# Optimization experiments

Measured on AMD Instinct MI355X. Metric: run time of the kernel, lower is better.

The kernel has to match this reference:

```python
import jax, jax.numpy as jnp
import numpy as np

N = 1048576
FEAT = 32
XRES = 512
TRES = 64
HID = 256
OUT = 2


def _bilinear_sample(plane, gx, gy):
    """plane: [C,H,W]; gx,gy: [N] in [-1,1] (x indexes W, y indexes H).
    Matches torch grid_sample(mode='bilinear', align_corners=True, padding_mode='zeros')
    for in-range coords. Returns [N,C]."""
    C, H, W = plane.shape
    ix = (gx + 1.0) * 0.5 * (W - 1)
    iy = (gy + 1.0) * 0.5 * (H - 1)
    x0f = jnp.floor(ix)
    y0f = jnp.floor(iy)
    wx = ix - x0f  # frac weights (grad flows to coords through ix)
    wy = iy - y0f
    x0 = jnp.clip(x0f.astype(jnp.int32), 0, W - 1)
    x1 = jnp.clip(x0 + 1, 0, W - 1)
    y0 = jnp.clip(y0f.astype(jnp.int32), 0, H - 1)
    y1 = jnp.clip(y0 + 1, 0, H - 1)
    v00 = plane[:, y0, x0]  # [C,N]
    v01 = plane[:, y0, x1]
    v10 = plane[:, y1, x0]
    v11 = plane[:, y1, x1]
    out = (v00 * ((1 - wx) * (1 - wy)) + v01 * (wx * (1 - wy))
           + v10 * ((1 - wx) * wy) + v11 * (wx * wy))
    return out.T  # [N,C]


def setup_inputs() -> dict:
    key = jax.random.key(0)
    ks = jax.random.split(key, 12)
    coords = jax.random.uniform(ks[0], (N, 3), jnp.float32, minval=-1.0, maxval=1.0)
    xy_plane = jax.random.normal(ks[1], (FEAT, XRES, XRES), jnp.float32) * 0.001
    yt_plane = jax.random.normal(ks[2], (FEAT, TRES, XRES), jnp.float32) * 0.001
    xt_plane = jax.random.normal(ks[3], (FEAT, TRES, XRES), jnp.float32) * 0.001
    def lin(kw, kb, fan_in, fan_out):
        bound = 1.0 / np.sqrt(fan_in)
        w = jax.random.uniform(kw, (fan_in, fan_out), jnp.float32, -bound, bound)
        b = jax.random.uniform(kb, (fan_out,), jnp.float32, -bound, bound)
        return w, b
    w1, b1 = lin(ks[4], ks[5], FEAT, HID)
    w2, b2 = lin(ks[6], ks[7], HID, HID)
    w3, b3 = lin(ks[8], ks[9], HID, HID)
    w4, b4 = lin(ks[10], ks[11], HID, OUT)
    return {"coordinates": coords, "xy_plane": xy_plane, "yt_plane": yt_plane,
            "xt_plane": xt_plane, "w1": w1, "b1": b1, "w2": w2, "b2": b2,
            "w3": w3, "b3": b3, "w4": w4, "b4": b4}


def reference(coordinates, xy_plane, yt_plane, xt_plane,
              w1, b1, w2, b2, w3, b3, w4, b4):
    x, y, t = coordinates[:, 0], coordinates[:, 1], coordinates[:, 2]
    # coords[...,0:2] -> xy plane; coords[...,1:3] -> yt plane; coords[...,::2] -> xt plane
    feats = (_bilinear_sample(xy_plane, x, y)
             + _bilinear_sample(yt_plane, y, t)
             + _bilinear_sample(xt_plane, x, t))  # [N, FEAT]
    h = jax.nn.leaky_relu(feats @ w1 + b1, 0.01)
    h = jax.nn.leaky_relu(h @ w2 + b2, 0.01)
    h = jax.nn.leaky_relu(h @ w3 + b3, 0.01)
    out = jax.nn.sigmoid(h @ w4 + b4)  # [N, OUT]
    return out
```

## Files before the change

### kernel.cpp

```cpp
#include <hip/hip_runtime.h>

typedef unsigned short u16;
typedef float f32x4 __attribute__((ext_vector_type(4)));
typedef short short8 __attribute__((ext_vector_type(8)));
typedef short short4v __attribute__((ext_vector_type(4)));

#define XRES 512
#define TRES 64

#define WS_XY 0
#define WS_YT 8388608
#define WS_XT 9437184
#define WS_WF 10485760
#define WF1 0
#define WF2 8192
#define WF3 73728
#define WS_NEEDED_BYTES 21250048ull

__device__ __forceinline__ u16 f2bf(float f) {
  union { float f; unsigned u; } v; v.f = f;
  unsigned r = v.u + 0x7FFFu + ((v.u >> 16) & 1u);
  return (u16)(r >> 16);
}
__device__ __forceinline__ float bf2f(u16 u) {
  union { unsigned u; float f; } v; v.u = ((unsigned)u) << 16;
  return v.f;
}

__device__ __forceinline__ f32x4 mfma16x16x32_bf16(short8 a, short8 b, f32x4 c) {
  f32x4 d;
  asm("v_mfma_f32_16x16x32_bf16 %0, %1, %2, %3" : "=v"(d) : "v"(a), "v"(b), "v"(c));
  return d;
}

__device__ __forceinline__ void sample_direct(const float* __restrict__ pl, int H, int W,
                                              float gx, float gy, float* acc) {
  float ix = (gx + 1.0f) * 0.5f * (float)(W - 1);
  float iy = (gy + 1.0f) * 0.5f * (float)(H - 1);
  float x0f = floorf(ix), y0f = floorf(iy);
  float wx = ix - x0f, wy = iy - y0f;
  int x0 = (int)x0f, y0 = (int)y0f;
  x0 = max(0, min(x0, W - 1)); y0 = max(0, min(y0, H - 1));
  int x1 = min(x0 + 1, W - 1), y1 = min(y0 + 1, H - 1);
  float w00 = (1.0f - wx) * (1.0f - wy), w01 = wx * (1.0f - wy);
  float w10 = (1.0f - wx) * wy,          w11 = wx * wy;
  const int HW = H * W;
  const int i00 = y0 * W + x0, i01 = y0 * W + x1, i10 = y1 * W + x0, i11 = y1 * W + x1;
#pragma unroll
  for (int c = 0; c < 32; ++c) {
    const float* pc = pl + c * HW;
    acc[c] += w00 * pc[i00] + w01 * pc[i01] + w10 * pc[i10] + w11 * pc[i11];
  }
}

__device__ void layer_valu(const float* hin, float* hout, const float* __restrict__ w,
                           const float* __restrict__ b) {
  for (int pass = 0; pass < 8; ++pass) {
    float acc[32];
#pragma unroll
    for (int jx = 0; jx < 32; ++jx) acc[jx] = b[pass * 32 + jx];
    for (int k = 0; k < 256; ++k) {
      const float hk = hin[k];
      const float* wr = w + k * 256 + pass * 32;
#pragma unroll
      for (int jx = 0; jx < 32; ++jx) acc[jx] = fmaf(hk, wr[jx], acc[jx]);
    }
#pragma unroll
    for (int jx = 0; jx < 32; ++jx) {
      float v = acc[jx];
      hout[pass * 32 + jx] = v > 0.f ? v : 0.01f * v;
    }
  }
}

__global__ void triplane_safe(const float* __restrict__ coords,
                              const float* __restrict__ xy, const float* __restrict__ yt,
                              const float* __restrict__ xt,
                              const float* __restrict__ w1, const float* __restrict__ b1,
                              const float* __restrict__ w2, const float* __restrict__ b2,
                              const float* __restrict__ w3, const float* __restrict__ b3,
                              const float* __restrict__ w4, const float* __restrict__ b4,
                              float* __restrict__ out) {
  const int pg = blockIdx.x * 256 + threadIdx.x;
  const float x  = coords[pg * 3 + 0];
  const float y  = coords[pg * 3 + 1];
  const float tt = coords[pg * 3 + 2];
  float feats[32];
#pragma unroll
  for (int c = 0; c < 32; ++c) feats[c] = 0.f;
  sample_direct(xy, XRES, XRES, x, y,  feats);
  sample_direct(yt, TRES, XRES, y, tt, feats);
  sample_direct(xt, TRES, XRES, x, tt, feats);

  float hA[256], hB[256];
  for (int pass = 0; pass < 8; ++pass) {
    float acc[32];
#pragma unroll
    for (int jx = 0; jx < 32; ++jx) acc[jx] = b1[pass * 32 + jx];
#pragma unroll
    for (int k = 0; k < 32; ++k) {
      const float fk = feats[k];
      const float* wr = w1 + k * 256 + pass * 32;
#pragma unroll
      for (int jx = 0; jx < 32; ++jx) acc[jx] = fmaf(fk, wr[jx], acc[jx]);
    }
#pragma unroll
    for (int jx = 0; jx < 32; ++jx) {
      float v = acc[jx];
      hA[pass * 32 + jx] = v > 0.f ? v : 0.01f * v;
    }
  }
  layer_valu(hA, hB, w2, b2);
  layer_valu(hB, hA, w3, b3);
  float a0 = b4[0], a1 = b4[1];
  for (int k = 0; k < 256; ++k) {
    a0 = fmaf(hA[k], w4[k * 2 + 0], a0);
    a1 = fmaf(hA[k], w4[k * 2 + 1], a1);
  }
  out[pg * 2 + 0] = 1.f / (1.f + __expf(-a0));
  out[pg * 2 + 1] = 1.f / (1.f + __expf(-a1));
}

__global__ void prep_planes(const float* __restrict__ xy, const float* __restrict__ yt,
                            const float* __restrict__ xt, u16* __restrict__ ws) {
  int i = blockIdx.x * 256 + threadIdx.x;
  const float* src; u16* dst; int HW; int idx;
  if (i < 262144)      { src = xy; dst = ws + WS_XY; HW = 262144; idx = i; }
  else if (i < 294912) { src = yt; dst = ws + WS_YT; HW = 32768;  idx = i - 262144; }
  else                 { src = xt; dst = ws + WS_XT; HW = 32768;  idx = i - 294912; }
  u16 tmp[32];
#pragma unroll
  for (int c = 0; c < 32; ++c) tmp[c] = f2bf(src[c * HW + idx]);
  short8* o = (short8*)(dst + (long)idx * 32);
#pragma unroll
  for (int s = 0; s < 4; ++s) o[s] = *(short8*)(tmp + s * 8);
}

__global__ void prep_weights(const float* __restrict__ w1, const float* __restrict__ w2,
                             const float* __restrict__ w3, u16* __restrict__ wf) {
  int tid = blockIdx.x * 256 + threadIdx.x;
  const float* src; int KS; int local; int dstbase;
  if (tid < 1024)      { src = w1; KS = 1; local = tid;        dstbase = WF1; }
  else if (tid < 9216) { src = w2; KS = 8; local = tid - 1024; dstbase = WF2; }
  else                 { src = w3; KS = 8; local = tid - 9216; dstbase = WF3; }
  int lane = local & 63, blk = local >> 6;
  int ks = blk % KS, CT = blk / KS;
  int col = CT * 16 + (lane & 15);
  int kb = ks * 32 + (lane >> 4) * 8;
  u16 tmp[8];
#pragma unroll
  for (int j = 0; j < 8; ++j) tmp[j] = f2bf(src[(kb + j) * 256 + col]);
  *(short8*)(wf + dstbase + local * 8) = *(short8*)tmp;
}

__device__ __forceinline__ void sample_plane4(const u16* __restrict__ pl, int H, int W,
                                              float gx, float gy, int c0, float* acc) {
  float ix = (gx + 1.0f) * 0.5f * (float)(W - 1);
  float iy = (gy + 1.0f) * 0.5f * (float)(H - 1);
  float x0f = floorf(ix), y0f = floorf(iy);
  float wx = ix - x0f, wy = iy - y0f;
  int x0 = (int)x0f, y0 = (int)y0f;
  x0 = max(0, min(x0, W - 1)); y0 = max(0, min(y0, H - 1));
  int x1 = min(x0 + 1, W - 1);
  int y1 = min(y0 + 1, H - 1);
  short4v v00 = *(const short4v*)(pl + (y0 * W + x0) * 32 + c0);
  short4v v01 = *(const short4v*)(pl + (y0 * W + x1) * 32 + c0);
  short4v v10 = *(const short4v*)(pl + (y1 * W + x0) * 32 + c0);
  short4v v11 = *(const short4v*)(pl + (y1 * W + x1) * 32 + c0);
  float w00 = (1.0f - wx) * (1.0f - wy), w01 = wx * (1.0f - wy);
  float w10 = (1.0f - wx) * wy,          w11 = wx * wy;
#pragma unroll
  for (int j = 0; j < 4; ++j)
    acc[j] += w00 * bf2f((u16)v00[j]) + w01 * bf2f((u16)v01[j])
            + w10 * bf2f((u16)v10[j]) + w11 * bf2f((u16)v11[j]);
}

template <int KSTEPS>
__device__ __forceinline__ void layer_gemm(const u16* src, u16* dst,
                                           const u16* __restrict__ wf,
                                           const float* __restrict__ bias,
                                           int wave, int lane) {
  const int r16 = lane & 15, kq = lane >> 4;
  f32x4 acc[2][4];
#pragma unroll
  for (int rt = 0; rt < 2; ++rt)
#pragma unroll
    for (int ct = 0; ct < 4; ++ct) acc[rt][ct] = (f32x4){0.f, 0.f, 0.f, 0.f};

  short8 aA[2], aB[2], bA[4], bB[4];

#define LDA(ks, dst_)                                                                   \
  {                                                                                     \
    const int kbyte_ = (ks) * 64 + kq * 16;                                             \
    _Pragma("unroll") for (int rt = 0; rt < 2; ++rt) {                                  \
      const int row_ = rt * 16 + r16;                                                   \
      dst_[rt] = *(const short8*)((const char*)src + row_ * 512 +                       \
                                  (kbyte_ ^ ((row_ & 7) << 4)));                        \
    }                                                                                   \
  }
#define LDB(ks, dst_)                                                                   \
  {                                                                                     \
    _Pragma("unroll") for (int ct = 0; ct < 4; ++ct)                                    \
        dst_[ct] = *(const short8*)(wf + (((wave * 4 + ct) * KSTEPS + (ks)) * 64 +      \
                                          lane) * 8);                                   \
  }

  LDA(0, aA); LDB(0, bA);
#pragma unroll
  for (int ks = 0; ks < KSTEPS; ++ks) {
    const bool even = (ks & 1) == 0;
    short8* ac = even ? aA : aB;
    short8* bc = even ? bA : bB;
    short8* an = even ? aB : aA;
    short8* bn = even ? bB : bA;
    if (ks + 1 < KSTEPS) { LDA(ks + 1, an); LDB(ks + 1, bn); }
#pragma unroll
    for (int rt = 0; rt < 2; ++rt)
#pragma unroll
      for (int ct = 0; ct < 4; ++ct)
        acc[rt][ct] = mfma16x16x32_bf16(ac[rt], bc[ct], acc[rt][ct]);
  }
#undef LDA
#undef LDB

#pragma unroll
  for (int ct = 0; ct < 4; ++ct) {
    const int col = wave * 64 + ct * 16 + r16;
    const float bv = bias[col];
#pragma unroll
    for (int rt = 0; rt < 2; ++rt)
#pragma unroll
      for (int q = 0; q < 4; ++q) {
        const int row = rt * 16 + kq * 4 + q;
        float v = acc[rt][ct][q] + bv;
        v = v > 0.f ? v : 0.01f * v;
        *(u16*)((char*)dst + row * 512 + ((col * 2) ^ ((row & 7) << 4))) = f2bf(v);
      }
  }
}

__global__ __launch_bounds__(256, 4) void triplane_fused(
    const float* __restrict__ coords, const u16* __restrict__ ws,
    const float* __restrict__ b1, const float* __restrict__ b2,
    const float* __restrict__ b3, const float* __restrict__ w4,
    const float* __restrict__ b4, float* __restrict__ out) {
  __shared__ u16 sA[32 * 256];
  __shared__ u16 sB[32 * 256];
  const int t = threadIdx.x;
  const int lane = t & 63, wave = t >> 6;
  const int pg0 = blockIdx.x * 32;

  {
    const int p = t >> 3, cg = t & 7, c0 = cg * 4;
    const int pg = pg0 + p;
    const float x  = coords[pg * 3 + 0];
    const float y  = coords[pg * 3 + 1];
    const float tt = coords[pg * 3 + 2];
    float acc4[4] = {0.f, 0.f, 0.f, 0.f};
    sample_plane4(ws + WS_XY, XRES, XRES, x, y,  c0, acc4);
    sample_plane4(ws + WS_YT, TRES, XRES, y, tt, c0, acc4);
    sample_plane4(ws + WS_XT, TRES, XRES, x, tt, c0, acc4);
    u16 packed[4];
#pragma unroll
    for (int j = 0; j < 4; ++j) packed[j] = f2bf(acc4[j]);
    *(short4v*)((char*)sA + p * 512 + ((c0 * 2) ^ ((p & 7) << 4))) = *(short4v*)packed;
  }
  __syncthreads();

  const u16* wfb = ws + WS_WF;
  layer_gemm<1>(sA, sB, wfb + WF1, b1, wave, lane);
  __syncthreads();
  layer_gemm<8>(sB, sA, wfb + WF2, b2, wave, lane);
  __syncthreads();
  layer_gemm<8>(sA, sB, wfb + WF3, b3, wave, lane);
  __syncthreads();

  {
    const int p = t >> 3, cg = t & 7;
    const int pg = pg0 + p;
    float a0 = 0.f, a1 = 0.f;
#pragma unroll
    for (int kk = 0; kk < 4; ++kk) {
      const int k0 = cg * 32 + kk * 8;
      short8 h = *(const short8*)((const char*)sB + p * 512 + ((k0 * 2) ^ ((p & 7) << 4)));
#pragma unroll
      for (int j = 0; j < 8; ++j) {
        const float hv = bf2f((u16)h[j]);
        a0 = fmaf(hv, w4[(k0 + j) * 2 + 0], a0);
        a1 = fmaf(hv, w4[(k0 + j) * 2 + 1], a1);
      }
    }
    a0 += __shfl_xor(a0, 1, 8); a0 += __shfl_xor(a0, 2, 8); a0 += __shfl_xor(a0, 4, 8);
    a1 += __shfl_xor(a1, 1, 8); a1 += __shfl_xor(a1, 2, 8); a1 += __shfl_xor(a1, 4, 8);
    if (cg == 0) {
      const float o0 = 1.f / (1.f + __expf(-(a0 + b4[0])));
      const float o1 = 1.f / (1.f + __expf(-(a1 + b4[1])));
      *(float2*)(out + pg * 2) = make_float2(o0, o1);
    }
  }
}

extern "C" void kernel_launch(void* const* d_in, const int* in_sizes, int n_in,
                              void* d_out, int out_size, void* d_ws, size_t ws_size,
                              hipStream_t stream) {
  (void)in_sizes; (void)n_in; (void)out_size;
  const float* coords = (const float*)d_in[0];
  const float* xy = (const float*)d_in[1];
  const float* yt = (const float*)d_in[2];
  const float* xt = (const float*)d_in[3];
  const float* w1 = (const float*)d_in[4];
  const float* b1 = (const float*)d_in[5];
  const float* w2 = (const float*)d_in[6];
  const float* b2 = (const float*)d_in[7];
  const float* w3 = (const float*)d_in[8];
  const float* b3 = (const float*)d_in[9];
  const float* w4 = (const float*)d_in[10];
  const float* b4 = (const float*)d_in[11];

  if (ws_size >= WS_NEEDED_BYTES && d_ws != nullptr) {
    u16* ws = (u16*)d_ws;
    prep_planes<<<1280, 256, 0, stream>>>(xy, yt, xt, ws);
    prep_weights<<<68, 256, 0, stream>>>(w1, w2, w3, ws + WS_WF);
    triplane_fused<<<32768, 256, 0, stream>>>(coords, ws, b1, b2, b3, w4, b4, (float*)d_out);
  } else {
    triplane_safe<<<4096, 256, 0, stream>>>(coords, xy, yt, xt, w1, b1, w2, b2, w3, b3, w4, b4,
                                            (float*)d_out);
  }
}
```

Before: 679.0 us.

## Double block to 64 points with 8 waves and retile layer GEMMs

Each block now handles 64 points with 512 threads instead of 32 points with 256 threads. The hidden-layer GEMM tile per wave changes from 32 rows × 64 columns to 64 rows × 32 columns, so each weight fragment is reused across more rows. The bias is folded into the accumulator initialisation, leaky ReLU becomes fmaxf, bf16 conversion uses the packed v_cvt_pk_bf16 instruction, and the MFMA uses the compiler builtin instead of inline asm. The price is double the LDS per block, which may limit occupancy, and the unseen parts of the kernel (later layers and output) must be consistent with 8 waves and 64 rows.

```diff
diff --git a/kernel.cpp b/kernel.cpp
--- a/kernel.cpp
+++ b/kernel.cpp
@@ -1,6 +1,7 @@
 #include <hip/hip_runtime.h>
 
 typedef unsigned short u16;
+typedef unsigned int u32;
 typedef float f32x4 __attribute__((ext_vector_type(4)));
 typedef short short8 __attribute__((ext_vector_type(8)));
 typedef short short4v __attribute__((ext_vector_type(4)));
@@ -26,11 +27,14 @@
   union { unsigned u; float f; } v; v.u = ((unsigned)u) << 16;
   return v.f;
 }
+__device__ __forceinline__ u32 cvtpk_bf16(float lo, float hi) {
+  u32 d;
+  asm("v_cvt_pk_bf16_f32 %0, %1, %2" : "=v"(d) : "v"(lo), "v"(hi));
+  return d;
+}
 
 __device__ __forceinline__ f32x4 mfma16x16x32_bf16(short8 a, short8 b, f32x4 c) {
-  f32x4 d;
-  asm("v_mfma_f32_16x16x32_bf16 %0, %1, %2, %3" : "=v"(d) : "v"(a), "v"(b), "v"(c));
-  return d;
+  return __builtin_amdgcn_mfma_f32_16x16x32_bf16(a, b, c, 0, 0, 0);
 }
 
 __device__ __forceinline__ void sample_direct(const float* __restrict__ pl, int H, int W,
@@ -181,18 +185,20 @@
                                            const float* __restrict__ bias,
                                            int wave, int lane) {
   const int r16 = lane & 15, kq = lane >> 4;
-  f32x4 acc[2][4];
-#pragma unroll
-  for (int rt = 0; rt < 2; ++rt)
-#pragma unroll
-    for (int ct = 0; ct < 4; ++ct) acc[rt][ct] = (f32x4){0.f, 0.f, 0.f, 0.f};
-
-  short8 aA[2], aB[2], bA[4], bB[4];
+  f32x4 acc[4][2];
+#pragma unroll
+  for (int ct = 0; ct < 2; ++ct) {
+    const float bv = bias[wave * 32 + ct * 16 + r16];
+#pragma unroll
+    for (int rt = 0; rt < 4; ++rt) acc[rt][ct] = (f32x4){bv, bv, bv, bv};
+  }
+
+  short8 aA[4], aB[4], bA[2], bB[2];
 
 #define LDA(ks, dst_)                                                                   \
   {                                                                                     \
     const int kbyte_ = (ks) * 64 + kq * 16;                                             \
-    _Pragma("unroll") for (int rt = 0; rt < 2; ++rt) {                                  \
+    _Pragma("unroll") for (int rt = 0; rt < 4; ++rt) {                                  \
       const int row_ = rt * 16 + r16;                                                   \
       dst_[rt] = *(const short8*)((const char*)src + row_ * 512 +                       \
                                   (kbyte_ ^ ((row_ & 7) << 4)));                        \
@@ -200,8 +206,8 @@
   }
 #define LDB(ks, dst_)                                                                   \
   {                                                                                     \
-    _Pragma("unroll") for (int ct = 0; ct < 4; ++ct)                                    \
-        dst_[ct] = *(const short8*)(wf + (((wave * 4 + ct) * KSTEPS + (ks)) * 64 +      \
+    _Pragma("unroll") for (int ct = 0; ct < 2; ++ct)                                    \
+        dst_[ct] = *(const short8*)(wf + (((wave * 2 + ct) * KSTEPS + (ks)) * 64 +      \
                                           lane) * 8);                                   \
   }
 
@@ -215,40 +221,45 @@
     short8* bn = even ? bB : bA;
     if (ks + 1 < KSTEPS) { LDA(ks + 1, an); LDB(ks + 1, bn); }
 #pragma unroll
-    for (int rt = 0; rt < 2; ++rt)
-#pragma unroll
-      for (int ct = 0; ct < 4; ++ct)
+    for (int rt = 0; rt < 4; ++rt)
+#pragma unroll
+      for (int ct = 0; ct < 2; ++ct)
         acc[rt][ct] = mfma16x16x32_bf16(ac[rt], bc[ct], acc[rt][ct]);
   }
 #undef LDA
 #undef LDB
 
 #pragma unroll
-  for (int ct = 0; ct < 4; ++ct) {
-    const int col = wave * 64 + ct * 16 + r16;
-    const float bv = bias[col];
-#pragma unroll
-    for (int rt = 0; rt < 2; ++rt)
-#pragma unroll
-      for (int q = 0; q < 4; ++q) {
-        const int row = rt * 16 + kq * 4 + q;
-        float v = acc[rt][ct][q] + bv;
-        v = v > 0.f ? v : 0.01f * v;
-        *(u16*)((char*)dst + row * 512 + ((col * 2) ^ ((row & 7) << 4))) = f2bf(v);
+  for (int ct = 0; ct < 2; ++ct) {
+    const int col = wave * 32 + ct * 16 + r16;
+#pragma unroll
+    for (int rt = 0; rt < 4; ++rt) {
+#pragma unroll
+      for (int qp = 0; qp < 2; ++qp) {
+        float v0 = acc[rt][ct][qp * 2 + 0];
+        float v1 = acc[rt][ct][qp * 2 + 1];
+        v0 = fmaxf(v0, 0.01f * v0);
+        v1 = fmaxf(v1, 0.01f * v1);
+        const u32 pk = cvtpk_bf16(v0, v1);
+        const int row0 = rt * 16 + kq * 4 + qp * 2;
+        const int row1 = row0 + 1;
+        *(u16*)((char*)dst + row0 * 512 + ((col * 2) ^ ((row0 & 7) << 4))) = (u16)pk;
+        *(u16*)((char*)dst + row1 * 512 + ((col * 2) ^ ((row1 & 7) << 4))) = (u16)(pk >> 16);
       }
-  }
-}
-
-__global__ __launch_bounds__(256, 4) void triplane_fused(
+    }
+  }
+}
+
+__global__ __launch_bounds__(512, 4) void triplane_fused(
     const float* __restrict__ coords, const u16* __restrict__ ws,
     const float* __restrict__ b1, const float* __restrict__ b2,
     const float* __restrict__ b3, const float* __restrict__ w4,
     const float* __restrict__ b4, float* __restrict__ out) {
-  __shared__ u16 sA[32 * 256];
-  __shared__ u16 sB[32 * 256];
+  __shared__ u16 sA[64 * 256];
+  __shared__ u16 sB[64 * 256];
   const int t = threadIdx.x;
   const int lane = t & 63, wave = t >> 6;
-  const int pg0 = blockIdx.x * 32;
+  const int pg0 = blockIdx.x * 64;
 
   {
     const int p = t >> 3, cg = t & 7, c0 = cg * 4;
@@ -321,7 +332,7 @@
     u16* ws = (u16*)d_ws;
     prep_planes<<<1280, 256, 0, stream>>>(xy, yt, xt, ws);
     prep_weights<<<68, 256, 0, stream>>>(w1, w2, w3, ws + WS_WF);
-    triplane_fused<<<32768, 256, 0, stream>>>(coords, ws, b1, b2, b3, w4, b4, (float*)d_out);
+    triplane_fused<<<16384, 512, 0, stream>>>(coords, ws, b1, b2, b3, w4, b4, (float*)d_out);
   } else {
     triplane_safe<<<4096, 256, 0, stream>>>(coords, xy, yt, xt, w1, b1, w2, b2, w3, b3, w4, b4,
                                             (float*)d_out);
```

After: 573.4 us. -15.6%, faster.

## Move final layer to MFMA, fold bias into accumulators, packed bf16 stores

Applied to the files above, without the earlier changes.

The 256-to-2 output layer now runs as a padded MFMA on two waves, using pre-converted bf16 w4 stored in the workspace, instead of scalar FMAs with shuffle reductions. Biases now initialise the accumulators instead of being added in the epilogue. Leaky-relu uses fmax and the bf16 conversion uses packed v_cvt_pk_bf16_f32. Layer-1 weights are prefetched before sampling to hide their load latency. The aim is to cut ALU and global-load work in the epilogues, at the cost of bf16 rounding in the last layer and idle waves there.

```diff
diff --git a/kernel.cpp b/kernel.cpp
--- a/kernel.cpp
+++ b/kernel.cpp
@@ -1,6 +1,7 @@
 #include <hip/hip_runtime.h>
 
 typedef unsigned short u16;
+typedef unsigned int u32;
 typedef float f32x4 __attribute__((ext_vector_type(4)));
 typedef short short8 __attribute__((ext_vector_type(8)));
 typedef short short4v __attribute__((ext_vector_type(4)));
@@ -15,7 +16,8 @@
 #define WF1 0
 #define WF2 8192
 #define WF3 73728
-#define WS_NEEDED_BYTES 21250048ull
+#define WF4 139264
+#define WS_NEEDED_BYTES 21258240ull
 
 __device__ __forceinline__ u16 f2bf(float f) {
   union { float f; unsigned u; } v; v.f = f;
@@ -26,11 +28,13 @@
   union { unsigned u; float f; } v; v.u = ((unsigned)u) << 16;
   return v.f;
 }
-
+__device__ __forceinline__ u32 cvtpk_bf16(float lo, float hi) {
+  u32 d;
+  asm("v_cvt_pk_bf16_f32 %0, %1, %2" : "=v"(d) : "v"(lo), "v"(hi));
+  return d;
+}
 __device__ __forceinline__ f32x4 mfma16x16x32_bf16(short8 a, short8 b, f32x4 c) {
-  f32x4 d;
-  asm("v_mfma_f32_16x16x32_bf16 %0, %1, %2, %3" : "=v"(d) : "v"(a), "v"(b), "v"(c));
-  return d;
+  return __builtin_amdgcn_mfma_f32_16x16x32_bf16(a, b, c, 0, 0, 0);
 }
 
 __device__ __forceinline__ void sample_direct(const float* __restrict__ pl, int H, int W,
@@ -137,20 +141,32 @@
 }
 
 __global__ void prep_weights(const float* __restrict__ w1, const float* __restrict__ w2,
-                             const float* __restrict__ w3, u16* __restrict__ wf) {
+                             const float* __restrict__ w3, const float* __restrict__ w4,
+                             u16* __restrict__ wf) {
   int tid = blockIdx.x * 256 + threadIdx.x;
-  const float* src; int KS; int local; int dstbase;
-  if (tid < 1024)      { src = w1; KS = 1; local = tid;        dstbase = WF1; }
-  else if (tid < 9216) { src = w2; KS = 8; local = tid - 1024; dstbase = WF2; }
-  else                 { src = w3; KS = 8; local = tid - 9216; dstbase = WF3; }
-  int lane = local & 63, blk = local >> 6;
-  int ks = blk % KS, CT = blk / KS;
-  int col = CT * 16 + (lane & 15);
-  int kb = ks * 32 + (lane >> 4) * 8;
-  u16 tmp[8];
-#pragma unroll
-  for (int j = 0; j < 8; ++j) tmp[j] = f2bf(src[(kb + j) * 256 + col]);
-  *(short8*)(wf + dstbase + local * 8) = *(short8*)tmp;
+  if (tid < 17408) {
+    const float* src; int KS; int local; int dstbase;
+    if (tid < 1024)      { src = w1; KS = 1; local = tid;        dstbase = WF1; }
+    else if (tid < 9216) { src = w2; KS = 8; local = tid - 1024; dstbase = WF2; }
+    else                 { src = w3; KS = 8; local = tid - 9216; dstbase = WF3; }
+    int lane = local & 63, blk = local >> 6;
+    int ks = blk % KS, CT = blk / KS;
+    int col = CT * 16 + (lane & 15);
+    int kb = ks * 32 + (lane >> 4) * 8;
+    u16 tmp[8];
+#pragma unroll
+    for (int j = 0; j < 8; ++j) tmp[j] = f2bf(src[(kb + j) * 256 + col]);
+    *(short8*)(wf + dstbase + local * 8) = *(short8*)tmp;
+  } else {
+    int local = tid - 17408;
+    int lane = local & 63, ks = local >> 6;
+    int col = lane & 15;
+    int kb = ks * 32 + (lane >> 4) * 8;
+    u16 tmp[8];
+#pragma unroll
+    for (int j = 0; j < 8; ++j) tmp[j] = (col < 2) ? f2bf(w4[(kb + j) * 2 + col]) : (u16)0;
+    *(short8*)(wf + WF4 + local * 8) = *(short8*)tmp;
+  }
 }
 
 __device__ __forceinline__ void sample_plane4(const u16* __restrict__ pl, int H, int W,
@@ -175,6 +191,29 @@
             + w10 * bf2f((u16)v10[j]) + w11 * bf2f((u16)v11[j]);
 }
 
+__device__ __forceinline__ void store_acts(f32x4 (&acc)[2][4], u16* dst, int wave,
+                                           int r16, int kq) {
+#pragma unroll
+  for (int ct = 0; ct < 4; ++ct) {
+    const int col = wave * 64 + ct * 16 + r16;
+#pragma unroll
+    for (int rt = 0; rt < 2; ++rt) {
+#pragma unroll
+      for (int qp = 0; qp < 2; ++qp) {
+        float v0 = acc[rt][ct][qp * 2 + 0];
+        float v1 = acc[rt][ct][qp * 2 + 1];
+        v0 = fmaxf(v0, 0.01f * v0);
+        v1 = fmaxf(v1, 0.01f * v1);
+        const u32 pk = cvtpk_bf16(v0, v1);
+        const int row0 = rt * 16 + kq * 4 + qp * 2;
+        const int row1 = row0 + 1;
+        *(u16*)((char*)dst + row0 * 512 + ((col * 2) ^ ((row0 & 7) << 4))) = (u16)pk;
+        *(u16*)((char*)dst + row1 * 512 + ((col * 2) ^ ((row1 & 7) << 4))) = (u16)(pk >> 16);
+      }
+    }
+  }
+}
+
 template <int KSTEPS>
 __device__ __forceinline__ void layer_gemm(const u16* src, u16* dst,
                                            const u16* __restrict__ wf,
@@ -183,9 +222,11 @@
   const int r16 = lane & 15, kq = lane >> 4;
   f32x4 acc[2][4];
 #pragma unroll
-  for (int rt = 0; rt < 2; ++rt)
-#pragma unroll
-    for (int ct = 0; ct < 4; ++ct) acc[rt][ct] = (f32x4){0.f, 0.f, 0.f, 0.f};
+  for (int ct = 0; ct < 4; ++ct) {
+    const float bv = bias[wave * 64 + ct * 16 + r16];
+#pragma unroll
+    for (int rt = 0; rt < 2; ++rt) acc[rt][ct] = (f32x4){bv, bv, bv, bv};
+  }
 
   short8 aA[2], aB[2], bA[4], bB[4];
 
@@ -223,32 +264,26 @@
 #undef LDA
 #undef LDB
 
-#pragma unroll
-  for (int ct = 0; ct < 4; ++ct) {
-    const int col = wave * 64 + ct * 16 + r16;
-    const float bv = bias[col];
-#pragma unroll
-    for (int rt = 0; rt < 2; ++rt)
-#pragma unroll
-      for (int q = 0; q < 4; ++q) {
-        const int row = rt * 16 + kq * 4 + q;
-        float v = acc[rt][ct][q] + bv;
-        v = v > 0.f ? v : 0.01f * v;
-        *(u16*)((char*)dst + row * 512 + ((col * 2) ^ ((row & 7) << 4))) = f2bf(v);
-      }
-  }
+  store_acts(acc, dst, wave, r16, kq);
 }
 
 __global__ __launch_bounds__(256, 4) void triplane_fused(
     const float* __restrict__ coords, const u16* __restrict__ ws,
     const float* __restrict__ b1, const float* __restrict__ b2,
-    const float* __restrict__ b3, const float* __restrict__ w4,
-    const float* __restrict__ b4, float* __restrict__ out) {
+    const float* __restrict__ b3, const float* __restrict__ b4,
+    float* __restrict__ out) {
   __shared__ u16 sA[32 * 256];
   __shared__ u16 sB[32 * 256];
   const int t = threadIdx.x;
   const int lane = t & 63, wave = t >> 6;
+  const int r16 = lane & 15, kq = lane >> 4;
   const int pg0 = blockIdx.x * 32;
+  const u16* wfb = ws + WS_WF;
+
+  short8 b1pre[4];
+#pragma unroll
+  for (int ct = 0; ct < 4; ++ct)
+    b1pre[ct] = *(const short8*)(wfb + WF1 + (((wave * 4 + ct) * 64 + lane) * 8));
 
   {
     const int p = t >> 3, cg = t & 7, c0 = cg * 4;
@@ -267,35 +302,52 @@
   }
   __syncthreads();
 
-  const u16* wfb = ws + WS_WF;
-  layer_gemm<1>(sA, sB, wfb + WF1, b1, wave, lane);
+  {
+    f32x4 acc[2][4];
+#pragma unroll
+    for (int ct = 0; ct < 4; ++ct) {
+      const float bv = b1[wave * 64 + ct * 16 + r16];
+#pragma unroll
+      for (int rt = 0; rt < 2; ++rt) acc[rt][ct] = (f32x4){bv, bv, bv, bv};
+    }
+    short8 a[2];
+    const int kbyte = kq * 16;
+#pragma unroll
+    for (int rt = 0; rt < 2; ++rt) {
+      const int row = rt * 16 + r16;
+      a[rt] = *(const short8*)((const char*)sA + row * 512 + (kbyte ^ ((row & 7) << 4)));
+    }
+#pragma unroll
+    for (int rt = 0; rt < 2; ++rt)
+#pragma unroll
+      for (int ct = 0; ct < 4; ++ct)
+        acc[rt][ct] = mfma16x16x32_bf16(a[rt], b1pre[ct], acc[rt][ct]);
+    store_acts(acc, sB, wave, r16, kq);
+  }
   __syncthreads();
   layer_gemm<8>(sB, sA, wfb + WF2, b2, wave, lane);
   __syncthreads();
   layer_gemm<8>(sA, sB, wfb + WF3, b3, wave, lane);
   __syncthreads();
 
-  {
-    const int p = t >> 3, cg = t & 7;
-    const int pg = pg0 + p;
-    float a0 = 0.f, a1 = 0.f;
-#pragma unroll
-    for (int kk = 0; kk < 4; ++kk) {
-      const int k0 = cg * 32 + kk * 8;
-      short8 h = *(const short8*)((const char*)sB + p * 512 + ((k0 * 2) ^ ((p & 7) << 4)));
-#pragma unroll
-      for (int j = 0; j < 8; ++j) {
-        const float hv = bf2f((u16)h[j]);
-        a0 = fmaf(hv, w4[(k0 + j) * 2 + 0], a0);
-        a1 = fmaf(hv, w4[(k0 + j) * 2 + 1], a1);
+  if (wave < 2) {
+    f32x4 acc = (f32x4){0.f, 0.f, 0.f, 0.f};
+#pragma unroll
+    for (int ks = 0; ks < 8; ++ks) {
+      const int kbyte = ks * 64 + kq * 16;
+      const int row = wave * 16 + r16;
+      short8 a = *(const short8*)((const char*)sB + row * 512 + (kbyte ^ ((row & 7) << 4)));
+      short8 b = *(const short8*)(wfb + WF4 + (ks * 64 + lane) * 8);
+      acc = mfma16x16x32_bf16(a, b, acc);
+    }
+    if (r16 < 2) {
+      const float bv = b4[r16];
+#pragma unroll
+      for (int q = 0; q < 4; ++q) {
+        const int row = wave * 16 + kq * 4 + q;
+        const float o = 1.f / (1.f + __expf(-(acc[q] + bv)));
+        out[(pg0 + row) * 2 + r16] = o;
       }
-    }
-    a0 += __shfl_xor(a0, 1, 8); a0 += __shfl_xor(a0, 2, 8); a0 += __shfl_xor(a0, 4, 8);
-    a1 += __shfl_xor(a1, 1, 8); a1 += __shfl_xor(a1, 2, 8); a1 += __shfl_xor(a1, 4, 8);
-    if (cg == 0) {
-      const float o0 = 1.f / (1.f + __expf(-(a0 + b4[0])));
-      const float o1 = 1.f / (1.f + __expf(-(a1 + b4[1])));
-      *(float2*)(out + pg * 2) = make_float2(o0, o1);
     }
   }
 }
@@ -320,8 +372,8 @@
   if (ws_size >= WS_NEEDED_BYTES && d_ws != nullptr) {
     u16* ws = (u16*)d_ws;
     prep_planes<<<1280, 256, 0, stream>>>(xy, yt, xt, ws);
-    prep_weights<<<68, 256, 0, stream>>>(w1, w2, w3, ws + WS_WF);
-    triplane_fused<<<32768, 256, 0, stream>>>(coords, ws, b1, b2, b3, w4, b4, (float*)d_out);
+    prep_weights<<<70, 256, 0, stream>>>(w1, w2, w3, w4, ws + WS_WF);
+    triplane_fused<<<32768, 256, 0, stream>>>(coords, ws, b1, b2, b3, b4, (float*)d_out);
   } else {
     triplane_safe<<<4096, 256, 0, stream>>>(coords, xy, yt, xt, w1, b1, w2, b2, w3, b3, w4, b4,
                                             (float*)d_out);
```

After: 751.3 us. +10.7%, slower.

## Double block tile to 64 points with 8 waves and permuted packed epilogue

Applied to the files above, without the earlier changes.

Each block now handles 64 points with 512 threads, and the 8 waves are split into two row halves by four column groups. Each B-fragment load from global weights is therefore reused by two waves' worth of rows per block, halving weight traffic per point. The GEMM epilogue folds the bias into the accumulator init and uses fmax for leaky ReLU. Outputs are packed with v_cvt_pk_bf16 into 32-bit LDS stores in a permuted column order, and the weights of the next layer (w2, w3, w4) are pre-permuted on the host-side prep kernel to match. LDS per block doubles to 64KB, which may limit occupancy, and the new launch bound asks for 512 threads × 4 blocks.

```diff
diff --git a/kernel.cpp b/kernel.cpp
--- a/kernel.cpp
+++ b/kernel.cpp
@@ -1,6 +1,7 @@
 #include <hip/hip_runtime.h>
 
 typedef unsigned short u16;
+typedef unsigned int u32;
 typedef float f32x4 __attribute__((ext_vector_type(4)));
 typedef short short8 __attribute__((ext_vector_type(8)));
 typedef short short4v __attribute__((ext_vector_type(4)));
@@ -15,7 +16,12 @@
 #define WF1 0
 #define WF2 8192
 #define WF3 73728
-#define WS_NEEDED_BYTES 21250048ull
+#define WF4 139264
+#define WS_NEEDED_BYTES 21258240ull
+
+__host__ __device__ __forceinline__ int slot2col(int p) {
+  return ((p >> 6) << 6) + ((p & 3) << 4) + ((p >> 2) & 15);
+}
 
 __device__ __forceinline__ u16 f2bf(float f) {
   union { float f; unsigned u; } v; v.f = f;
@@ -26,12 +32,15 @@
   union { unsigned u; float f; } v; v.u = ((unsigned)u) << 16;
   return v.f;
 }
-
+__device__ __forceinline__ u32 cvtpk_bf16(float lo, float hi) {
+  u32 d;
+  asm("v_cvt_pk_bf16_f32 %0, %1, %2" : "=v"(d) : "v"(lo), "v"(hi));
+  return d;
+}
 __device__ __forceinline__ f32x4 mfma16x16x32_bf16(short8 a, short8 b, f32x4 c) {
-  f32x4 d;
-  asm("v_mfma_f32_16x16x32_bf16 %0, %1, %2, %3" : "=v"(d) : "v"(a), "v"(b), "v"(c));
-  return d;
-}
+  return __builtin_amdgcn_mfma_f32_16x16x32_bf16(a, b, c, 0, 0, 0);
+}
+__device__ __forceinline__ float leaky(float v) { return fmaxf(v, 0.01f * v); }
 
 __device__ __forceinline__ void sample_direct(const float* __restrict__ pl, int H, int W,
                                               float gx, float gy, float* acc) {
@@ -137,20 +146,35 @@
 }
 
 __global__ void prep_weights(const float* __restrict__ w1, const float* __restrict__ w2,
-                             const float* __restrict__ w3, u16* __restrict__ wf) {
+                             const float* __restrict__ w3, const float* __restrict__ w4,
+                             u16* __restrict__ wf) {
   int tid = blockIdx.x * 256 + threadIdx.x;
-  const float* src; int KS; int local; int dstbase;
-  if (tid < 1024)      { src = w1; KS = 1; local = tid;        dstbase = WF1; }
-  else if (tid < 9216) { src = w2; KS = 8; local = tid - 1024; dstbase = WF2; }
-  else                 { src = w3; KS = 8; local = tid - 9216; dstbase = WF3; }
-  int lane = local & 63, blk = local >> 6;
-  int ks = blk % KS, CT = blk / KS;
-  int col = CT * 16 + (lane & 15);
-  int kb = ks * 32 + (lane >> 4) * 8;
-  u16 tmp[8];
-#pragma unroll
-  for (int j = 0; j < 8; ++j) tmp[j] = f2bf(src[(kb + j) * 256 + col]);
-  *(short8*)(wf + dstbase + local * 8) = *(short8*)tmp;
+  if (tid < 1024) {
+    int local = tid, lane = local & 63, CT = local >> 6;
+    int col = CT * 16 + (lane & 15);
+    int kb = (lane >> 4) * 8;
+    u16 tmp[8];
+#pragma unroll
+    for (int j = 0; j < 8; ++j) tmp[j] = f2bf(w1[(kb + j) * 256 + col]);
+    *(short8*)(wf + WF1 + local * 8) = *(short8*)tmp;
+  } else if (tid < 17408) {
+    const float* src; int local; int dstbase;
+    if (tid < 9216) { src = w2; local = tid - 1024; dstbase = WF2; }
+    else            { src = w3; local = tid - 9216; dstbase = WF3; }
+    int lane = local & 63, blk = local >> 6;
+    int ks = blk % 8, CT = blk / 8;
+    int col = CT * 16 + (lane & 15);
+    int kb = ks * 32 + (lane >> 4) * 8;
+    u16 tmp[8];
+#pragma unroll
+    for (int j = 0; j < 8; ++j) tmp[j] = f2bf(src[slot2col(kb + j) * 256 + col]);
+    *(short8*)(wf + dstbase + local * 8) = *(short8*)tmp;
+  } else if (tid < 17664) {
+    int p = tid - 17408;
+    float* w4p = (float*)(wf + WF4);
+    w4p[p * 2 + 0] = w4[slot2col(p) * 2 + 0];
+    w4p[p * 2 + 1] = w4[slot2col(p) * 2 + 1];
+  }
 }
 
 __device__ __forceinline__ void sample_plane4(const u16* __restrict__ pl, int H, int W,
@@ -181,11 +205,15 @@
                                            const float* __restrict__ bias,
                                            int wave, int lane) {
   const int r16 = lane & 15, kq = lane >> 4;
+  const int rh = (wave & 1) * 32;
+  const int wc = wave >> 1;
   f32x4 acc[2][4];
 #pragma unroll
-  for (int rt = 0; rt < 2; ++rt)
-#pragma unroll
-    for (int ct = 0; ct < 4; ++ct) acc[rt][ct] = (f32x4){0.f, 0.f, 0.f, 0.f};
+  for (int ct = 0; ct < 4; ++ct) {
+    const float bv = bias[wc * 64 + ct * 16 + r16];
+#pragma unroll
+    for (int rt = 0; rt < 2; ++rt) acc[rt][ct] = (f32x4){bv, bv, bv, bv};
+  }
 
   short8 aA[2], aB[2], bA[4], bB[4];
 
@@ -193,7 +221,7 @@
   {                                                                                     \
     const int kbyte_ = (ks) * 64 + kq * 16;                                             \
     _Pragma("unroll") for (int rt = 0; rt < 2; ++rt) {                                  \
-      const int row_ = rt * 16 + r16;                                                   \
+      const int row_ = rh + rt * 16 + r16;                                              \
       dst_[rt] = *(const short8*)((const char*)src + row_ * 512 +                       \
                                   (kbyte_ ^ ((row_ & 7) << 4)));                        \
     }                                                                                   \
@@ -201,7 +229,7 @@
 #define LDB(ks, dst_)                                                                   \
   {                                                                                     \
     _Pragma("unroll") for (int ct = 0; ct < 4; ++ct)                                    \
-        dst_[ct] = *(const short8*)(wf + (((wave * 4 + ct) * KSTEPS + (ks)) * 64 +      \
+        dst_[ct] = *(const short8*)(wf + (((wc * 4 + ct) * KSTEPS + (ks)) * 64 +        \
                                           lane) * 8);                                   \
   }
 
@@ -224,31 +252,31 @@
 #undef LDB
 
 #pragma unroll
-  for (int ct = 0; ct < 4; ++ct) {
-    const int col = wave * 64 + ct * 16 + r16;
-    const float bv = bias[col];
-#pragma unroll
-    for (int rt = 0; rt < 2; ++rt)
-#pragma unroll
-      for (int q = 0; q < 4; ++q) {
-        const int row = rt * 16 + kq * 4 + q;
-        float v = acc[rt][ct][q] + bv;
-        v = v > 0.f ? v : 0.01f * v;
-        *(u16*)((char*)dst + row * 512 + ((col * 2) ^ ((row & 7) << 4))) = f2bf(v);
-      }
-  }
-}
-
-__global__ __launch_bounds__(256, 4) void triplane_fused(
+  for (int rt = 0; rt < 2; ++rt) {
+#pragma unroll
+    for (int q = 0; q < 4; ++q) {
+      const int row = rh + rt * 16 + kq * 4 + q;
+      const int swz = (row & 7) << 4;
+      const u32 pk0 = cvtpk_bf16(leaky(acc[rt][0][q]), leaky(acc[rt][1][q]));
+      const u32 pk1 = cvtpk_bf16(leaky(acc[rt][2][q]), leaky(acc[rt][3][q]));
+      char* base = (char*)dst + row * 512;
+      *(u32*)(base + ((wc * 128 + r16 * 8 + 0) ^ swz)) = pk0;
+      *(u32*)(base + ((wc * 128 + r16 * 8 + 4) ^ swz)) = pk1;
+    }
+  }
+}
+
+__global__ __launch_bounds__(512, 4) void triplane_fused(
     const float* __restrict__ coords, const u16* __restrict__ ws,
     const float* __restrict__ b1, const float* __restrict__ b2,
-    const float* __restrict__ b3, const float* __restrict__ w4,
-    const float* __restrict__ b4, float* __restrict__ out) {
-  __shared__ u16 sA[32 * 256];
-  __shared__ u16 sB[32 * 256];
+    const float* __restrict__ b3, const float* __restrict__ b4,
+    float* __restrict__ out) {
+  __shared__ u16 sA[64 * 256];
+  __shared__ u16 sB[64 * 256];
   const int t = threadIdx.x;
   const int lane = t & 63, wave = t >> 6;
-  const int pg0 = blockIdx.x * 32;
+  const int pg0 = blockIdx.x * 64;
+  const u16* wfb = ws + WS_WF;
 
   {
     const int p = t >> 3, cg = t & 7, c0 = cg * 4;
@@ -267,7 +295,6 @@
   }
   __syncthreads();
 
-  const u16* wfb = ws + WS_WF;
   layer_gemm<1>(sA, sB, wfb + WF1, b1, wave, lane);
   __syncthreads();
   layer_gemm<8>(sB, sA, wfb + WF2, b2, wave, lane);
@@ -278,16 +305,19 @@
   {
     const int p = t >> 3, cg = t & 7;
     const int pg = pg0 + p;
+    const float* w4p = (const float*)(wfb + WF4);
     float a0 = 0.f, a1 = 0.f;
 #pragma unroll
-    for (int kk = 0; kk < 4; ++kk) {
-      const int k0 = cg * 32 + kk * 8;
-      short8 h = *(const short8*)((const char*)sB + p * 512 + ((k0 * 2) ^ ((p & 7) << 4)));
+    for (int i = 0; i < 4; ++i) {
+      short8 h = *(const short8*)((const char*)sB + p * 512 +
+                                  ((cg * 64 + i * 16) ^ ((p & 7) << 4)));
+      const int s0 = cg * 32 + i * 8;
 #pragma unroll
       for (int j = 0; j < 8; ++j) {
         const float hv = bf2f((u16)h[j]);
-        a0 = fmaf(hv, w4[(k0 + j) * 2 + 0], a0);
-        a1 = fmaf(hv, w4[(k0 + j) * 2 + 1], a1);
+        const float2 wv = *(const float2*)(w4p + (s0 + j) * 2);
+        a0 = fmaf(hv, wv.x, a0);
+        a1 = fmaf(hv, wv.y, a1);
       }
     }
     a0 += __shfl_xor(a0, 1, 8); a0 += __shfl_xor(a0, 2, 8); a0 += __shfl_xor(a0, 4, 8);
@@ -320,8 +350,8 @@
   if (ws_size >= WS_NEEDED_BYTES && d_ws != nullptr) {
     u16* ws = (u16*)d_ws;
     prep_planes<<<1280, 256, 0, stream>>>(xy, yt, xt, ws);
-    prep_weights<<<68, 256, 0, stream>>>(w1, w2, w3, ws + WS_WF);
-    triplane_fused<<<32768, 256, 0, stream>>>(coords, ws, b1, b2, b3, w4, b4, (float*)d_out);
+    prep_weights<<<70, 256, 0, stream>>>(w1, w2, w3, w4, ws + WS_WF);
+    triplane_fused<<<16384, 512, 0, stream>>>(coords, ws, b1, b2, b3, b4, (float*)d_out);
   } else {
     triplane_safe<<<4096, 256, 0, stream>>>(coords, xy, yt, xt, w1, b1, w2, b2, w3, b3, w4, b4,
                                             (float*)d_out);
```

Result: faster. 632.7 us (-6.8%).
